# Optimization experiments

Hardware: AMD Instinct MI355X
Metric: run time of the kernel (lower is better)

The kernel has to match this reference:

```python
import jax, jax.numpy as jnp
import numpy as np

B, T, C = 4, 2048, 1024
H = 16
DH = C // H


def setup_inputs() -> dict:
    key = jax.random.key(0)
    k1, k2, k3 = jax.random.split(key, 3)
    x = jax.random.normal(k1, (B, T, C), dtype=jnp.float32)
    w_qkv = jax.random.normal(k2, (3 * C, C), dtype=jnp.float32) * (1.0 / np.sqrt(C))
    w_out = jax.random.normal(k3, (C, C), dtype=jnp.float32) * (1.0 / np.sqrt(C))
    attn_mask = jnp.ones((B, T), dtype=jnp.int32)
    return {"x": x, "attn_mask": attn_mask, "w_qkv": w_qkv, "w_out": w_out}


def reference(x, attn_mask, w_qkv, w_out):
    b, t, c = x.shape
    h, dh = H, DH
    qkv = jnp.einsum('btc,fc->btf', x, w_qkv)  # [B,T,3C]
    q, k, v = jnp.split(qkv, 3, axis=-1)
    # [B,H,T,Dh]
    q = q.reshape(b, t, h, dh).transpose(0, 2, 1, 3)
    k = k.reshape(b, t, h, dh).transpose(0, 2, 1, 3)
    v = v.reshape(b, t, h, dh).transpose(0, 2, 1, 3)
    scale = jnp.sqrt(jnp.float32(dh))
    scores = jnp.einsum('bhqd,bhkd->bhqk', q, k) / scale  # [B,H,T,T]
    causal = jnp.tril(jnp.ones((t, t), dtype=bool))
    mask = causal[None, None, :, :] & (attn_mask[:, None, None, :] != 0)
    scores = jnp.where(mask, scores, -jnp.inf)
    p = jax.nn.softmax(scores, axis=-1)
    p = jnp.where(jnp.isnan(p), 0.0, p)  # nan_to_num for fully-masked rows
    out = jnp.einsum('bhqk,bhkd->bhqd', p, v)
    out = out.transpose(0, 2, 1, 3).reshape(b, t, c)
    return jnp.einsum('btc,fc->btf', out, w_out)
```

## Files before the change

### kernel.cpp

```cpp
#include <hip/hip_runtime.h>
#include <cstdint>
#include <cmath>


#define Bb 4
#define Tt 2048
#define Cc 1024
#define Hh 16
#define DHd 64
#define Mm (Bb*Tt)

typedef __attribute__((ext_vector_type(8))) short bf16x8;
typedef __attribute__((ext_vector_type(4))) short s16x4;
typedef __attribute__((ext_vector_type(4))) float f32x4;
typedef __attribute__((ext_vector_type(2))) unsigned int u32x2;

__device__ __forceinline__ short f2bf(float f) {
  uint32_t u = __builtin_bit_cast(uint32_t, f);
  u = (u + 0x7fffu + ((u >> 16) & 1u)) >> 16;
  return (short)(uint16_t)u;
}

__device__ __forceinline__ uint32_t cvtpk(float lo, float hi) {
  uint32_t r;
  asm("v_cvt_pk_bf16_f32 %0, %1, %2" : "=v"(r) : "v"(lo), "v"(hi));
  return r;
}

__global__ void cvt_bf16(const float* __restrict__ in, short* __restrict__ out, int n4) {
  int i = blockIdx.x * blockDim.x + threadIdx.x;
  if (i >= n4) return;
  f32x4 v = reinterpret_cast<const f32x4*>(in)[i];
  s16x4 o;
  o.x = f2bf(v.x); o.y = f2bf(v.y); o.z = f2bf(v.z); o.w = f2bf(v.w);
  reinterpret_cast<s16x4*>(out)[i] = o;
}

#define BK 32

template<int MODE>
__global__ __launch_bounds__(256) void gemm_bt(
    const short* __restrict__ A, const short* __restrict__ Bt, int K, int N,
    float* __restrict__ Cout,
    short* __restrict__ qb, short* __restrict__ kb, short* __restrict__ vtb)
{
  __shared__ __align__(16) short As[128*BK];
  __shared__ __align__(16) short Bs[128*BK];
  const int tid = threadIdx.x;
  const int lane = tid & 63, wid = tid >> 6;
  const int wr = wid >> 1, wc = wid & 1;
  const int bm = blockIdx.y, bn = blockIdx.x;
  const int r16 = lane & 15, g = lane >> 4;

  f32x4 acc[4][4];
#pragma unroll
  for (int i = 0; i < 4; ++i)
#pragma unroll
    for (int j = 0; j < 4; ++j) acc[i][j] = (f32x4)0.0f;

  const int srow = lane >> 2;
  const int scol = (lane & 3) * 8;
  const int ch0 = wid * 2;

  const int nk = K / BK;
  for (int kt = 0; kt < nk; ++kt) {
    const int k0 = kt * BK;
#pragma unroll
    for (int c = 0; c < 2; ++c) {
      const int chunk = ch0 + c;
      const int row = chunk * 16 + srow;
      const short* ga = A  + (size_t)(bm*128 + row)*K + k0 + scol;
      const short* gb = Bt + (size_t)(bn*128 + row)*K + k0 + scol;
      __builtin_amdgcn_global_load_lds((const __attribute__((address_space(1))) void*)ga,
                                       (__attribute__((address_space(3))) void*)(&As[chunk*512]), 16, 0, 0);
      __builtin_amdgcn_global_load_lds((const __attribute__((address_space(1))) void*)gb,
                                       (__attribute__((address_space(3))) void*)(&Bs[chunk*512]), 16, 0, 0);
    }
    __syncthreads();

    bf16x8 af[4], bfv[4];
#pragma unroll
    for (int mi = 0; mi < 4; ++mi)
      af[mi] = *reinterpret_cast<const bf16x8*>(&As[(wr*64 + mi*16 + r16)*BK + g*8]);
#pragma unroll
    for (int ni = 0; ni < 4; ++ni)
      bfv[ni] = *reinterpret_cast<const bf16x8*>(&Bs[(wc*64 + ni*16 + r16)*BK + g*8]);
#pragma unroll
    for (int mi = 0; mi < 4; ++mi)
#pragma unroll
      for (int ni = 0; ni < 4; ++ni)
        acc[mi][ni] = __builtin_amdgcn_mfma_f32_16x16x32_bf16(af[mi], bfv[ni], acc[mi][ni], 0, 0, 0);
    __syncthreads();
  }

#pragma unroll
  for (int mi = 0; mi < 4; ++mi) {
    const int row0 = bm*128 + wr*64 + mi*16 + g*4;
#pragma unroll
    for (int ni = 0; ni < 4; ++ni) {
      const int col_g = bn*128 + wc*64 + ni*16 + r16;
      if (MODE == 1) {
#pragma unroll
        for (int r = 0; r < 4; ++r)
          Cout[(size_t)(row0 + r) * N + col_g] = acc[mi][ni][r];
      } else {
        const int which = col_g >> 10;
        const int hd = col_g & 1023;
        const int h = hd >> 6, d = hd & 63;
        const int b = row0 >> 11, t0 = row0 & 2047;
        const int bh = b*Hh + h;
        if (which == 0) {
#pragma unroll
          for (int r = 0; r < 4; ++r)
            qb[(((size_t)bh*Tt + t0 + r) << 6) + d] = f2bf(acc[mi][ni][r] * 0.18033688f);
        } else if (which == 1) {
#pragma unroll
          for (int r = 0; r < 4; ++r)
            kb[(((size_t)bh*Tt + t0 + r) << 6) + d] = f2bf(acc[mi][ni][r]);
        } else {
          u32x2 w;
          w.x = cvtpk(acc[mi][ni][0], acc[mi][ni][1]);
          w.y = cvtpk(acc[mi][ni][2], acc[mi][ni][3]);
          *reinterpret_cast<u32x2*>(vtb + ((size_t)bh*DHd + d)*Tt + t0) = w;
        }
      }
    }
  }
}

__global__ __launch_bounds__(256) void attn_fwd(
    const short* __restrict__ qbf, const short* __restrict__ kbf,
    const short* __restrict__ vtb, const int* __restrict__ am,
    short* __restrict__ ob)
{
  __shared__ __align__(16) short Ks[2][64*64];
  __shared__ __align__(16) short Vts[2][64*64];
  __shared__ __align__(16) short Ps[128*72];
  const int tid = threadIdx.x;
  const int lane = tid & 63, wid = tid >> 6;
  const int r16 = lane & 15, g = lane >> 4;
  const int bh = blockIdx.x;
  const int b = bh >> 4, h = bh & 15;
  const int grp = blockIdx.y >> 2, rem = blockIdx.y & 3;
  const int qi = (grp == 0) ? 15 - rem : (grp == 1) ? rem : (grp == 2) ? 11 - rem : 4 + rem;
  const int q0 = qi * 128;
  const int wq0 = q0 + wid * 32;

  bf16x8 qf[2][2];
#pragma unroll
  for (int m = 0; m < 2; ++m) {
    const short* qbase = qbf + ((size_t)bh*Tt + wq0 + m*16 + r16)*DHd;
    qf[m][0] = *reinterpret_cast<const bf16x8*>(qbase + g*8);
    qf[m][1] = *reinterpret_cast<const bf16x8*>(qbase + 32 + g*8);
  }

  f32x4 o[2][4];
  float mrow[2], lrow[2];
#pragma unroll
  for (int m = 0; m < 2; ++m) {
    mrow[m] = -INFINITY; lrow[m] = 0.f;
#pragma unroll
    for (int i = 0; i < 4; ++i) o[m][i] = (f32x4)0.0f;
  }

  char* Pw = (char*)Ps + (wid*32 + r16)*144;
  const int nkv = 2*qi + 2;

  const int srow = tid >> 3, scc = tid & 7;
  bf16x8 kr[2], vr[2];
#pragma unroll
  for (int c = 0; c < 2; ++c) {
    const int row = srow + c*32;
    kr[c] = *reinterpret_cast<const bf16x8*>(kbf + ((size_t)bh*Tt + row)*DHd + scc*8);
    vr[c] = *reinterpret_cast<const bf16x8*>(vtb + ((size_t)bh*DHd + row)*Tt + scc*8);
  }
#pragma unroll
  for (int c = 0; c < 2; ++c) {
    const int row = srow + c*32;
    const int off = (row*128 + scc*16) ^ ((row & 7) << 4);
    *reinterpret_cast<bf16x8*>((char*)Ks[0] + off) = kr[c];
    *reinterpret_cast<bf16x8*>((char*)Vts[0] + off) = vr[c];
  }
  __syncthreads();

  for (int kv = 0; kv < nkv; ++kv) {
    const int cur = kv & 1;
    const int kv0 = kv * 64;
    const unsigned long long mb = __ballot(am[b*Tt + kv0 + lane] != 0);
    if (kv + 1 < nkv) {
#pragma unroll
      for (int c = 0; c < 2; ++c) {
        const int row = srow + c*32;
        kr[c] = *reinterpret_cast<const bf16x8*>(kbf + ((size_t)bh*Tt + kv0 + 64 + row)*DHd + scc*8);
        vr[c] = *reinterpret_cast<const bf16x8*>(vtb + ((size_t)bh*DHd + row)*Tt + kv0 + 64 + scc*8);
      }
    }

    if (kv0 <= wq0 + 31) {
      const char* kbp = (const char*)Ks[cur];
      const char* vbp = (const char*)Vts[cur];
      const int swzr = (r16 & 7) << 4;

      f32x4 st[2][4];
      __builtin_amdgcn_s_setprio(1);
#pragma unroll
      for (int kt = 0; kt < 4; ++kt) {
        const int rb = (kt*16 + r16)*128;
        const bf16x8 ka0 = *reinterpret_cast<const bf16x8*>(kbp + ((rb + g*16) ^ swzr));
        const bf16x8 ka1 = *reinterpret_cast<const bf16x8*>(kbp + ((rb + 64 + g*16) ^ swzr));
#pragma unroll
        for (int m = 0; m < 2; ++m) {
          f32x4 t = (f32x4)0.0f;
          t = __builtin_amdgcn_mfma_f32_16x16x32_bf16(ka0, qf[m][0], t, 0, 0, 0);
          t = __builtin_amdgcn_mfma_f32_16x16x32_bf16(ka1, qf[m][1], t, 0, 0, 0);
          st[m][kt] = t;
        }
      }
      __builtin_amdgcn_s_setprio(0);

      const bool notall = (mb != ~0ull);
      const bool diag = (kv0 + 63 > wq0);
      if (diag || notall) {
#pragma unroll
        for (int m = 0; m < 2; ++m) {
          const int qrow = wq0 + m*16 + r16;
#pragma unroll
          for (int kt = 0; kt < 4; ++kt)
#pragma unroll
            for (int r = 0; r < 4; ++r) {
              const int kl = kt*16 + g*4 + r;
              bool ok = !diag || (kv0 + kl <= qrow);
              if (notall) ok = ok && ((mb >> kl) & 1ull);
              if (!ok) st[m][kt][r] = -3.0e38f;
            }
        }
      }

      float mx[2], rs[2];
#pragma unroll
      for (int m = 0; m < 2; ++m) {
        f32x4 t0, t1;
#pragma unroll
        for (int i = 0; i < 4; ++i) { t0[i] = fmaxf(st[m][0][i], st[m][1][i]); t1[i] = fmaxf(st[m][2][i], st[m][3][i]); }
#pragma unroll
        for (int i = 0; i < 4; ++i) t0[i] = fmaxf(t0[i], t1[i]);
        mx[m] = fmaxf(fmaxf(t0[0], t0[1]), fmaxf(t0[2], t0[3]));
      }
      {
        float a0 = __shfl_xor(mx[0], 16), a1 = __shfl_xor(mx[1], 16);
        mx[0] = fmaxf(mx[0], a0); mx[1] = fmaxf(mx[1], a1);
        a0 = __shfl_xor(mx[0], 32); a1 = __shfl_xor(mx[1], 32);
        mx[0] = fmaxf(mx[0], a0); mx[1] = fmaxf(mx[1], a1);
      }
      const bool need = __any((mx[0] > mrow[0] + 8.f) || (mx[1] > mrow[1] + 8.f));
      if (need) {
#pragma unroll
        for (int m = 0; m < 2; ++m) {
          const float mnew = fmaxf(mrow[m], mx[m]);
          const float alpha = __builtin_amdgcn_exp2f(mrow[m] - mnew);
          mrow[m] = mnew;
          lrow[m] *= alpha;
#pragma unroll
          for (int dt = 0; dt < 4; ++dt) o[m][dt] *= alpha;
        }
      }

#pragma unroll
      for (int m = 0; m < 2; ++m) {
#pragma unroll
        for (int kt = 0; kt < 4; ++kt)
#pragma unroll
          for (int r = 0; r < 4; ++r)
            st[m][kt][r] = __builtin_amdgcn_exp2f(st[m][kt][r] - mrow[m]);
        char* pw = Pw + m*2304;
#pragma unroll
        for (int kt = 0; kt < 4; ++kt) {
          u32x2 w;
          w.x = cvtpk(st[m][kt][0], st[m][kt][1]);
          w.y = cvtpk(st[m][kt][2], st[m][kt][3]);
          *reinterpret_cast<u32x2*>(pw + kt*32 + g*8) = w;
        }
        f32x4 s4;
#pragma unroll
        for (int i = 0; i < 4; ++i) s4[i] = st[m][0][i] + st[m][1][i] + st[m][2][i] + st[m][3][i];
        rs[m] = (s4[0] + s4[1]) + (s4[2] + s4[3]);
      }
      {
        float a0 = __shfl_xor(rs[0], 16), a1 = __shfl_xor(rs[1], 16);
        rs[0] += a0; rs[1] += a1;
        a0 = __shfl_xor(rs[0], 32); a1 = __shfl_xor(rs[1], 32);
        rs[0] += a0; rs[1] += a1;
      }
      lrow[0] += rs[0]; lrow[1] += rs[1];

      __builtin_amdgcn_sched_barrier(0);

      __builtin_amdgcn_s_setprio(1);
#pragma unroll
      for (int ks = 0; ks < 2; ++ks) {
        const bf16x8 pb0 = *reinterpret_cast<const bf16x8*>(Pw + ks*64 + g*16);
        const bf16x8 pb1 = *reinterpret_cast<const bf16x8*>(Pw + 2304 + ks*64 + g*16);
#pragma unroll
        for (int dt = 0; dt < 4; ++dt) {
          const int rb = (dt*16 + r16)*128;
          const bf16x8 va = *reinterpret_cast<const bf16x8*>(vbp + ((rb + ks*64 + g*16) ^ swzr));
          o[0][dt] = __builtin_amdgcn_mfma_f32_16x16x32_bf16(va, pb0, o[0][dt], 0, 0, 0);
          o[1][dt] = __builtin_amdgcn_mfma_f32_16x16x32_bf16(va, pb1, o[1][dt], 0, 0, 0);
        }
      }
      __builtin_amdgcn_s_setprio(0);
    }

    if (kv + 1 < nkv) {
#pragma unroll
      for (int c = 0; c < 2; ++c) {
        const int row = srow + c*32;
        const int off = (row*128 + scc*16) ^ ((row & 7) << 4);
        *reinterpret_cast<bf16x8*>((char*)Ks[cur^1] + off) = kr[c];
        *reinterpret_cast<bf16x8*>((char*)Vts[cur^1] + off) = vr[c];
      }
    }
    __syncthreads();
  }

#pragma unroll
  for (int m = 0; m < 2; ++m) {
    const float inv = (mrow[m] > -1e37f) ? 1.0f / lrow[m] : 0.f;
    short* obase = ob + ((size_t)(b*Tt + wq0 + m*16 + r16))*Cc + h*DHd;
#pragma unroll
    for (int dt = 0; dt < 4; ++dt) {
      u32x2 w;
      w.x = cvtpk(o[m][dt][0]*inv, o[m][dt][1]*inv);
      w.y = cvtpk(o[m][dt][2]*inv, o[m][dt][3]*inv);
      *reinterpret_cast<u32x2*>(obase + dt*16 + g*4) = w;
    }
  }
}

extern "C" void kernel_launch(void* const* d_in, const int* in_sizes, int n_in,
                              void* d_out, int out_size, void* d_ws, size_t ws_size,
                              hipStream_t stream) {
  const float* x    = (const float*)d_in[0];
  const int*   am   = (const int*)d_in[1];
  const float* wqkv = (const float*)d_in[2];
  const float* wout = (const float*)d_in[3];
  float* out = (float*)d_out;

  const size_t mc = (size_t)Mm * Cc;
  short* ws    = (short*)d_ws;
  short* xb    = ws;
  short* wqkvb = xb + mc;
  short* woutb = wqkvb + (size_t)3*Cc*Cc;
  short* qbuf  = woutb + (size_t)Cc*Cc;
  short* kbuf  = qbuf + mc;
  short* vtbuf = kbuf + mc;
  short* attnb = xb;

  cvt_bf16<<<(int)((mc/4 + 255)/256), 256, 0, stream>>>(x, xb, (int)(mc/4));
  cvt_bf16<<<(3*Cc*Cc/4 + 255)/256, 256, 0, stream>>>(wqkv, wqkvb, 3*Cc*Cc/4);
  cvt_bf16<<<(Cc*Cc/4 + 255)/256, 256, 0, stream>>>(wout, woutb, Cc*Cc/4);

  gemm_bt<0><<<dim3(3*Cc/128, Mm/128), 256, 0, stream>>>(
      xb, wqkvb, Cc, 3*Cc, nullptr, qbuf, kbuf, vtbuf);

  attn_fwd<<<dim3(Bb*Hh, Tt/128), 256, 0, stream>>>(qbuf, kbuf, vtbuf, am, attnb);

  gemm_bt<1><<<dim3(Cc/128, Mm/128), 256, 0, stream>>>(
      attnb, woutb, Cc, Cc, out, nullptr, nullptr, nullptr);
}
```

Before: 223.8 us.

## Keep P in registers via 16x16x16 MFMA and remap attention grid per XCD

The softmax probabilities no longer take a round trip through shared memory. They stay in registers and feed 16x16x16 bf16 MFMAs directly, since the score accumulator layout matches that instruction's B-operand layout. This removes the P LDS write/read and the 18KB Ps buffer, at the cost of twice as many, smaller MFMAs and narrower V reads from LDS. Separately, the 2D grid is flattened to 1D, and block indices are remapped so that the eight heads sharing an XCD stay co-resident, which is meant to improve L2 reuse of K/V.

```diff
diff --git a/kernel.cpp b/kernel.cpp
--- a/kernel.cpp
+++ b/kernel.cpp
@@ -25,6 +25,18 @@
   uint32_t r;
   asm("v_cvt_pk_bf16_f32 %0, %1, %2" : "=v"(r) : "v"(lo), "v"(hi));
   return r;
+}
+
+__device__ __forceinline__ f32x4 mfma16(s16x4 a, s16x4 b, f32x4 c) {
+#if __has_builtin(__builtin_amdgcn_mfma_f32_16x16x16_bf16)
+  return __builtin_amdgcn_mfma_f32_16x16x16_bf16(a, b, c, 0, 0, 0);
+#elif __has_builtin(__builtin_amdgcn_mfma_f32_16x16x16bf16_1k)
+  return __builtin_amdgcn_mfma_f32_16x16x16bf16_1k(a, b, c, 0, 0, 0);
+#else
+  f32x4 d;
+  asm("v_mfma_f32_16x16x16_bf16 %0, %1, %2, %3" : "=v"(d) : "v"(a), "v"(b), "v"(c));
+  return d;
+#endif
 }
 
 __global__ void cvt_bf16(const float* __restrict__ in, short* __restrict__ out, int n4) {
@@ -135,14 +147,18 @@
 {
   __shared__ __align__(16) short Ks[2][64*64];
   __shared__ __align__(16) short Vts[2][64*64];
-  __shared__ __align__(16) short Ps[128*72];
   const int tid = threadIdx.x;
   const int lane = tid & 63, wid = tid >> 6;
   const int r16 = lane & 15, g = lane >> 4;
-  const int bh = blockIdx.x;
+
+  const int lin = blockIdx.x;
+  const int xcd = lin & 7;
+  const int idx = lin >> 3;
+  const int bh  = xcd * 8 + (idx & 7);
+  const int qi_raw = idx >> 3;
+  const int grp = qi_raw >> 2, rem = qi_raw & 3;
+  const int qi = (grp == 0) ? 15 - rem : (grp == 1) ? rem : (grp == 2) ? 11 - rem : 4 + rem;
   const int b = bh >> 4, h = bh & 15;
-  const int grp = blockIdx.y >> 2, rem = blockIdx.y & 3;
-  const int qi = (grp == 0) ? 15 - rem : (grp == 1) ? rem : (grp == 2) ? 11 - rem : 4 + rem;
   const int q0 = qi * 128;
   const int wq0 = q0 + wid * 32;
 
@@ -163,9 +179,7 @@
     for (int i = 0; i < 4; ++i) o[m][i] = (f32x4)0.0f;
   }
 
-  char* Pw = (char*)Ps + (wid*32 + r16)*144;
   const int nkv = 2*qi + 2;
-
   const int srow = tid >> 3, scc = tid & 7;
   bf16x8 kr[2], vr[2];
 #pragma unroll
@@ -265,6 +279,7 @@
         }
       }
 
+      s16x4 pb[2][4];
 #pragma unroll
       for (int m = 0; m < 2; ++m) {
 #pragma unroll
@@ -272,13 +287,12 @@
 #pragma unroll
           for (int r = 0; r < 4; ++r)
             st[m][kt][r] = __builtin_amdgcn_exp2f(st[m][kt][r] - mrow[m]);
-        char* pw = Pw + m*2304;
 #pragma unroll
         for (int kt = 0; kt < 4; ++kt) {
           u32x2 w;
           w.x = cvtpk(st[m][kt][0], st[m][kt][1]);
           w.y = cvtpk(st[m][kt][2], st[m][kt][3]);
-          *reinterpret_cast<u32x2*>(pw + kt*32 + g*8) = w;
+          pb[m][kt] = __builtin_bit_cast(s16x4, w);
         }
         f32x4 s4;
 #pragma unroll
@@ -293,19 +307,18 @@
       }
       lrow[0] += rs[0]; lrow[1] += rs[1];
 
-      __builtin_amdgcn_sched_barrier(0);
-
       __builtin_amdgcn_s_setprio(1);
 #pragma unroll
-      for (int ks = 0; ks < 2; ++ks) {
-        const bf16x8 pb0 = *reinterpret_cast<const bf16x8*>(Pw + ks*64 + g*16);
-        const bf16x8 pb1 = *reinterpret_cast<const bf16x8*>(Pw + 2304 + ks*64 + g*16);
-#pragma unroll
-        for (int dt = 0; dt < 4; ++dt) {
-          const int rb = (dt*16 + r16)*128;
-          const bf16x8 va = *reinterpret_cast<const bf16x8*>(vbp + ((rb + ks*64 + g*16) ^ swzr));
-          o[0][dt] = __builtin_amdgcn_mfma_f32_16x16x32_bf16(va, pb0, o[0][dt], 0, 0, 0);
-          o[1][dt] = __builtin_amdgcn_mfma_f32_16x16x32_bf16(va, pb1, o[1][dt], 0, 0, 0);
+      for (int dt = 0; dt < 4; ++dt) {
+        const int row = dt*16 + r16;
+        const int rb = row*128;
+        const int r7 = row & 7;
+#pragma unroll
+        for (int kt = 0; kt < 4; ++kt) {
+          const s16x4 va = *reinterpret_cast<const s16x4*>(
+              vbp + rb + ((((kt<<1) + (g>>1)) ^ r7) << 4) + (g & 1)*8);
+          o[0][dt] = mfma16(va, pb[0][kt], o[0][dt]);
+          o[1][dt] = mfma16(va, pb[1][kt], o[1][dt]);
         }
       }
       __builtin_amdgcn_s_setprio(0);
@@ -363,7 +376,7 @@
   gemm_bt<0><<<dim3(3*Cc/128, Mm/128), 256, 0, stream>>>(
       xb, wqkvb, Cc, 3*Cc, nullptr, qbuf, kbuf, vtbuf);
 
-  attn_fwd<<<dim3(Bb*Hh, Tt/128), 256, 0, stream>>>(qbuf, kbuf, vtbuf, am, attnb);
+  attn_fwd<<<dim3(Bb*Hh*Tt/128), 256, 0, stream>>>(qbuf, kbuf, vtbuf, am, attnb);
 
   gemm_bt<1><<<dim3(Cc/128, Mm/128), 256, 0, stream>>>(
       attnb, woutb, Cc, Cc, out, nullptr, nullptr, nullptr);
```

Result: faster. 218.3 us (-2.5%).
